# Optimization experiments

Hardware: AMD Instinct MI355X
Metric: run time of the kernel (lower is better)

The kernel has to match this reference:

```python
import jax, jax.numpy as jnp
import numpy as np

N_QUBITS = 4
DIM = 16  # 2**4 amplitudes
VOCAB = 40
SEQ = 1048576

# PennyLane default.qubit: wire 0 is the most-significant bit of the basis index.
_BITS = np.array([[(b >> (N_QUBITS - 1 - q)) & 1 for q in range(N_QUBITS)]
                  for b in range(DIM)], dtype=np.int32)          # [16, 4]
_POPCNT = _BITS.sum(axis=1)                                      # [16] int
_ZSIGN = (1 - 2 * _BITS).astype(np.float32)                      # [16, 4], +1 for |0>, -1 for |1>

def _cnot_perm(c, t):
    # basis permutation of CNOT(control=c, target=t); it is an involution
    idx = np.arange(DIM)
    ctrl = (idx >> (N_QUBITS - 1 - c)) & 1
    flipped = idx ^ (1 << (N_QUBITS - 1 - t))
    return np.where(ctrl == 1, flipped, idx)

_PERMS = [_cnot_perm(i, i + 1) for i in range(N_QUBITS - 1)]  # CNOT(0,1),(1,2),(2,3)


def setup_inputs() -> dict:
    key = jax.random.key(0)
    k1, k2, k3 = jax.random.split(key, 3)
    x = jax.random.uniform(k1, (1, SEQ), dtype=jnp.float32)
    q_weights = 0.01 * jax.random.normal(k2, (N_QUBITS,), dtype=jnp.float32)
    fc_weight = jax.random.normal(k3, (VOCAB, N_QUBITS), dtype=jnp.float32) / jnp.sqrt(4.0)
    fc_bias = jnp.zeros((VOCAB,), dtype=jnp.float32)
    return {"x": x, "q_weights": q_weights, "fc_weight": fc_weight, "fc_bias": fc_bias}


def reference(x, q_weights, fc_weight, fc_bias):
    theta = x[0]                      # [S] per-token angle, same on all 4 wires
    c = jnp.cos(theta * 0.5)
    s = jnp.sin(theta * 0.5)
    one = jnp.ones_like(c)
    # powers c^k, s^k for k=0..4 (avoids pow-grad issues at 0)
    cpow = jnp.stack([one, c, c * c, c * c * c, c * c * c * c], axis=-1)  # [S,5]
    spow = jnp.stack([one, s, s * s, s * s * s, s * s * s * s], axis=-1)  # [S,5]
    # product state of RY(theta)|0> on each wire: amp_b = c^(4-popcnt) * s^popcnt
    state = cpow[:, N_QUBITS - _POPCNT] * spow[:, _POPCNT]               # [S,16] real
    # apply the CNOT chain (basis permutations)
    for p in _PERMS:
        state = state[:, p]
    # RZ(w_q) on each wire contributes phase exp(-i*w_q*z_q/2)
    zs = jnp.asarray(_ZSIGN)                                              # [16,4]
    phase = jnp.exp(-0.5j * (zs @ q_weights.astype(jnp.float32)))         # [16] complex
    psi = state.astype(jnp.complex64) * phase                             # [S,16]
    probs = jnp.real(psi * jnp.conj(psi))                                 # [S,16]
    expvals = probs @ zs                                                  # [S,4] <Z_q>
    return expvals @ fc_weight.T + fc_bias                                # [S,VOCAB]
```

## Files before the change

kernel.cpp:

```cpp
#include <hip/hip_runtime.h>

#define THREADS 256

__global__ __launch_bounds__(THREADS) void sqm_kernel(
    const float* __restrict__ x,
    const float* __restrict__ fcw,
    const float* __restrict__ fcb,
    float* __restrict__ out,
    int n)
{
    const int Z[5][4] = {
        { 1, 1, 1, 1},
        { 2, 0,-2,-4},
        { 0,-2, 0, 6},
        {-2, 0, 2,-4},
        {-1, 1,-1, 1},
    };

    __shared__ __align__(16) float sA[5][40];
    __shared__ __align__(16) float sB[40];
    __shared__ float sU[THREADS * 5];

    const int t = threadIdx.x;

    if (t < 200) {
        const int k = t / 40, v = t % 40;
        float a = 0.f;
        #pragma unroll
        for (int q = 0; q < 4; ++q) a += (float)Z[k][q] * fcw[v * 4 + q];
        sA[k][v] = a;
    } else if (t < 240) {
        sB[t - 200] = fcb[t - 200];
    }

    const long long base = (long long)blockIdx.x * THREADS;
    const int i = (int)(base + t);
    const float theta = (i < n) ? x[i] : 0.f;
    const float C = 0.5f + 0.5f * __cosf(theta);
    const float S = 1.f - C;
    const float C2 = C * C, S2 = S * S, CS = C * S;
    sU[t * 5 + 0] = C2 * C2;
    sU[t * 5 + 1] = C2 * CS;
    sU[t * 5 + 2] = CS * CS;
    sU[t * 5 + 3] = CS * S2;
    sU[t * 5 + 4] = S2 * S2;
    __syncthreads();

    float4* __restrict__ out4 = reinterpret_cast<float4*>(out);
    const long long blockF4 = (long long)blockIdx.x * (THREADS * 10);
    const long long totalF4 = (long long)n * 10;
    #pragma unroll
    for (int kk = 0; kk < 10; ++kk) {
        const int j = t + kk * THREADS;
        const long long gj = blockF4 + j;
        if (gj < totalF4) {
            const int row = j / 10;
            const int c4  = (j - row * 10) * 4;
            const float u0 = sU[row * 5 + 0];
            const float u1 = sU[row * 5 + 1];
            const float u2 = sU[row * 5 + 2];
            const float u3 = sU[row * 5 + 3];
            const float u4 = sU[row * 5 + 4];
            const float4 a0 = *reinterpret_cast<const float4*>(&sA[0][c4]);
            const float4 a1 = *reinterpret_cast<const float4*>(&sA[1][c4]);
            const float4 a2 = *reinterpret_cast<const float4*>(&sA[2][c4]);
            const float4 a3 = *reinterpret_cast<const float4*>(&sA[3][c4]);
            const float4 a4 = *reinterpret_cast<const float4*>(&sA[4][c4]);
            const float4 b  = *reinterpret_cast<const float4*>(&sB[c4]);
            float4 r;
            r.x = b.x + u0*a0.x + u1*a1.x + u2*a2.x + u3*a3.x + u4*a4.x;
            r.y = b.y + u0*a0.y + u1*a1.y + u2*a2.y + u3*a3.y + u4*a4.y;
            r.z = b.z + u0*a0.z + u1*a1.z + u2*a2.z + u3*a3.z + u4*a4.z;
            r.w = b.w + u0*a0.w + u1*a1.w + u2*a2.w + u3*a3.w + u4*a4.w;
            out4[gj] = r;
        }
    }
}

extern "C" void kernel_launch(void* const* d_in, const int* in_sizes, int n_in,
                              void* d_out, int out_size, void* d_ws, size_t ws_size,
                              hipStream_t stream) {
    const float* x   = (const float*)d_in[0];
    const float* fcw = (const float*)d_in[2];
    const float* fcb = (const float*)d_in[3];
    float* out = (float*)d_out;
    const int n = in_sizes[0];
    const int grid = (n + THREADS - 1) / THREADS;
    hipLaunchKernelGGL(sqm_kernel, dim3(grid), dim3(THREADS), 0, stream,
                       x, fcw, fcb, out, n);
}
```

Baseline: 173.2 us.

## Vectorize per-row coefficient LDS layout, share sA loads across paired outputs, use nontemporal stores

Stores the five per-token coefficients as one 16-byte vector plus a separate scalar so each row needs two LDS reads instead of five. The output loop is restructured so each iteration handles two output float4s that share the same column (5*256 float4 apart is exactly 128 rows), letting the sA/sB loads be reused, and the per-element division is replaced by incremental row/column tracking. Output writes switch to nontemporal stores to avoid polluting cache for the large streaming output. This adds some index bookkeeping, and it depends on the pairing arithmetic staying correct.

```diff
diff --git a/kernel.cpp b/kernel.cpp
--- a/kernel.cpp
+++ b/kernel.cpp
@@ -1,6 +1,8 @@
 #include <hip/hip_runtime.h>
 
 #define THREADS 256
+
+typedef float f32x4 __attribute__((ext_vector_type(4)));
 
 __global__ __launch_bounds__(THREADS) void sqm_kernel(
     const float* __restrict__ x,
@@ -17,9 +19,10 @@
         {-1, 1,-1, 1},
     };
 
-    __shared__ __align__(16) float sA[5][40];
-    __shared__ __align__(16) float sB[40];
-    __shared__ float sU[THREADS * 5];
+    __shared__ __align__(16) float  sA[5][40];
+    __shared__ __align__(16) float  sB[40];
+    __shared__ __align__(16) f32x4  sU4[THREADS];
+    __shared__ float                sU5[THREADS];
 
     const int t = threadIdx.x;
 
@@ -39,41 +42,45 @@
     const float C = 0.5f + 0.5f * __cosf(theta);
     const float S = 1.f - C;
     const float C2 = C * C, S2 = S * S, CS = C * S;
-    sU[t * 5 + 0] = C2 * C2;
-    sU[t * 5 + 1] = C2 * CS;
-    sU[t * 5 + 2] = CS * CS;
-    sU[t * 5 + 3] = CS * S2;
-    sU[t * 5 + 4] = S2 * S2;
+    sU4[t] = (f32x4){C2 * C2, C2 * CS, CS * CS, CS * S2};
+    sU5[t] = S2 * S2;
     __syncthreads();
 
-    float4* __restrict__ out4 = reinterpret_cast<float4*>(out);
+    f32x4* __restrict__ out4 = reinterpret_cast<f32x4*>(out);
     const long long blockF4 = (long long)blockIdx.x * (THREADS * 10);
     const long long totalF4 = (long long)n * 10;
+
+    int row = t / 10;
+    int m   = t - row * 10;
     #pragma unroll
-    for (int kk = 0; kk < 10; ++kk) {
-        const int j = t + kk * THREADS;
-        const long long gj = blockF4 + j;
-        if (gj < totalF4) {
-            const int row = j / 10;
-            const int c4  = (j - row * 10) * 4;
-            const float u0 = sU[row * 5 + 0];
-            const float u1 = sU[row * 5 + 1];
-            const float u2 = sU[row * 5 + 2];
-            const float u3 = sU[row * 5 + 3];
-            const float u4 = sU[row * 5 + 4];
-            const float4 a0 = *reinterpret_cast<const float4*>(&sA[0][c4]);
-            const float4 a1 = *reinterpret_cast<const float4*>(&sA[1][c4]);
-            const float4 a2 = *reinterpret_cast<const float4*>(&sA[2][c4]);
-            const float4 a3 = *reinterpret_cast<const float4*>(&sA[3][c4]);
-            const float4 a4 = *reinterpret_cast<const float4*>(&sA[4][c4]);
-            const float4 b  = *reinterpret_cast<const float4*>(&sB[c4]);
-            float4 r;
-            r.x = b.x + u0*a0.x + u1*a1.x + u2*a2.x + u3*a3.x + u4*a4.x;
-            r.y = b.y + u0*a0.y + u1*a1.y + u2*a2.y + u3*a3.y + u4*a4.y;
-            r.z = b.z + u0*a0.z + u1*a1.z + u2*a2.z + u3*a3.z + u4*a4.z;
-            r.w = b.w + u0*a0.w + u1*a1.w + u2*a2.w + u3*a3.w + u4*a4.w;
-            out4[gj] = r;
+    for (int p = 0; p < 5; ++p) {
+        const int c4 = m * 4;
+        const long long gj0 = blockF4 + t + p * THREADS;
+        const long long gj1 = gj0 + 5 * THREADS;
+        const int rA = row, rB = row + 128;
+
+        const f32x4 a0 = *reinterpret_cast<const f32x4*>(&sA[0][c4]);
+        const f32x4 a1 = *reinterpret_cast<const f32x4*>(&sA[1][c4]);
+        const f32x4 a2 = *reinterpret_cast<const f32x4*>(&sA[2][c4]);
+        const f32x4 a3 = *reinterpret_cast<const f32x4*>(&sA[3][c4]);
+        const f32x4 a4 = *reinterpret_cast<const f32x4*>(&sA[4][c4]);
+        const f32x4 b  = *reinterpret_cast<const f32x4*>(&sB[c4]);
+
+        {
+            const f32x4 u = sU4[rA];
+            const float u4 = sU5[rA];
+            f32x4 r = b + u.x*a0 + u.y*a1 + u.z*a2 + u.w*a3 + u4*a4;
+            if (gj0 < totalF4) __builtin_nontemporal_store(r, out4 + gj0);
         }
+        {
+            const f32x4 u = sU4[rB];
+            const float u4 = sU5[rB];
+            f32x4 r = b + u.x*a0 + u.y*a1 + u.z*a2 + u.w*a3 + u4*a4;
+            if (gj1 < totalF4) __builtin_nontemporal_store(r, out4 + gj1);
+        }
+
+        row += 25; m += 6;
+        if (m >= 10) { m -= 10; row += 1; }
     }
 }
 
```

New measurement: 182.3 us. 5.3% more time.

## Rewrite output as Horner polynomial in S with 320-thread blocks

Applied to the files above, without the earlier changes.

Re-expresses the logits as a degree-4 polynomial in S = sin^2(theta/2), so each thread stores one scalar instead of five basis products and evaluates the result with Horner FMAs. The block size becomes 320, a multiple of 10 float4 chunks per row, so each thread keeps a fixed column group and loads its coefficients once, outside the loop. This removes the per-iteration divide/mod and the repeated LDS reads. The polynomial form can change rounding slightly, and 320 threads is five wave64s, which may affect occupancy.

```diff
diff --git a/kernel.cpp b/kernel.cpp
--- a/kernel.cpp
+++ b/kernel.cpp
@@ -1,6 +1,11 @@
 #include <hip/hip_runtime.h>
 
-#define THREADS 256
+#define THREADS 320
+#define ROWS_PER_BLOCK 320
+#define F4_PER_BLOCK 3200
+#define ITERS 10
+
+typedef float f32x4 __attribute__((ext_vector_type(4)));
 
 __global__ __launch_bounds__(THREADS) void sqm_kernel(
     const float* __restrict__ x,
@@ -9,71 +14,51 @@
     float* __restrict__ out,
     int n)
 {
-    const int Z[5][4] = {
-        { 1, 1, 1, 1},
-        { 2, 0,-2,-4},
-        { 0,-2, 0, 6},
-        {-2, 0, 2,-4},
-        {-1, 1,-1, 1},
-    };
-
-    __shared__ __align__(16) float sA[5][40];
-    __shared__ __align__(16) float sB[40];
-    __shared__ float sU[THREADS * 5];
+    __shared__ __align__(16) float sP[5][40];
+    __shared__ float sS[ROWS_PER_BLOCK];
 
     const int t = threadIdx.x;
 
-    if (t < 200) {
-        const int k = t / 40, v = t % 40;
-        float a = 0.f;
-        #pragma unroll
-        for (int q = 0; q < 4; ++q) a += (float)Z[k][q] * fcw[v * 4 + q];
-        sA[k][v] = a;
-    } else if (t < 240) {
-        sB[t - 200] = fcb[t - 200];
+    if (t < 40) {
+        const f32x4 w = *reinterpret_cast<const f32x4*>(&fcw[t * 4]);
+        const float b = fcb[t];
+        sP[0][t] = w.x + w.y + w.z + w.w + b;
+        sP[1][t] = -2.f*w.x - 4.f*w.y - 6.f*w.z - 8.f*w.w;
+        sP[2][t] =           4.f*w.y + 12.f*w.z + 24.f*w.w;
+        sP[3][t] =                     -8.f*w.z - 32.f*w.w;
+        sP[4][t] =                                16.f*w.w;
     }
 
-    const long long base = (long long)blockIdx.x * THREADS;
-    const int i = (int)(base + t);
+    const int i = blockIdx.x * ROWS_PER_BLOCK + t;
     const float theta = (i < n) ? x[i] : 0.f;
-    const float C = 0.5f + 0.5f * __cosf(theta);
-    const float S = 1.f - C;
-    const float C2 = C * C, S2 = S * S, CS = C * S;
-    sU[t * 5 + 0] = C2 * C2;
-    sU[t * 5 + 1] = C2 * CS;
-    sU[t * 5 + 2] = CS * CS;
-    sU[t * 5 + 3] = CS * S2;
-    sU[t * 5 + 4] = S2 * S2;
+    sS[t] = 0.5f - 0.5f * __cosf(theta);
     __syncthreads();
 
-    float4* __restrict__ out4 = reinterpret_cast<float4*>(out);
-    const long long blockF4 = (long long)blockIdx.x * (THREADS * 10);
+    const int m4 = (t % 10) * 4;
+    const f32x4 p0 = *reinterpret_cast<const f32x4*>(&sP[0][m4]);
+    const f32x4 p1 = *reinterpret_cast<const f32x4*>(&sP[1][m4]);
+    const f32x4 p2 = *reinterpret_cast<const f32x4*>(&sP[2][m4]);
+    const f32x4 p3 = *reinterpret_cast<const f32x4*>(&sP[3][m4]);
+    const f32x4 p4 = *reinterpret_cast<const f32x4*>(&sP[4][m4]);
+
+    f32x4* __restrict__ out4 = reinterpret_cast<f32x4*>(out);
+    const long long blockF4 = (long long)blockIdx.x * F4_PER_BLOCK;
     const long long totalF4 = (long long)n * 10;
+    int rloc = t / 10;
+
     #pragma unroll
-    for (int kk = 0; kk < 10; ++kk) {
-        const int j = t + kk * THREADS;
-        const long long gj = blockF4 + j;
+    for (int it = 0; it < ITERS; ++it) {
+        const long long gj = blockF4 + it * THREADS + t;
         if (gj < totalF4) {
-            const int row = j / 10;
-            const int c4  = (j - row * 10) * 4;
-            const float u0 = sU[row * 5 + 0];
-            const float u1 = sU[row * 5 + 1];
-            const float u2 = sU[row * 5 + 2];
-            const float u3 = sU[row * 5 + 3];
-            const float u4 = sU[row * 5 + 4];
-            const float4 a0 = *reinterpret_cast<const float4*>(&sA[0][c4]);
-            const float4 a1 = *reinterpret_cast<const float4*>(&sA[1][c4]);
-            const float4 a2 = *reinterpret_cast<const float4*>(&sA[2][c4]);
-            const float4 a3 = *reinterpret_cast<const float4*>(&sA[3][c4]);
-            const float4 a4 = *reinterpret_cast<const float4*>(&sA[4][c4]);
-            const float4 b  = *reinterpret_cast<const float4*>(&sB[c4]);
-            float4 r;
-            r.x = b.x + u0*a0.x + u1*a1.x + u2*a2.x + u3*a3.x + u4*a4.x;
-            r.y = b.y + u0*a0.y + u1*a1.y + u2*a2.y + u3*a3.y + u4*a4.y;
-            r.z = b.z + u0*a0.z + u1*a1.z + u2*a2.z + u3*a3.z + u4*a4.z;
-            r.w = b.w + u0*a0.w + u1*a1.w + u2*a2.w + u3*a3.w + u4*a4.w;
+            const float S = sS[rloc];
+            f32x4 r = p4;
+            r = r * S + p3;
+            r = r * S + p2;
+            r = r * S + p1;
+            r = r * S + p0;
             out4[gj] = r;
         }
+        rloc += 32;
     }
 }
 
@@ -85,7 +70,7 @@
     const float* fcb = (const float*)d_in[3];
     float* out = (float*)d_out;
     const int n = in_sizes[0];
-    const int grid = (n + THREADS - 1) / THREADS;
+    const int grid = (n + ROWS_PER_BLOCK - 1) / ROWS_PER_BLOCK;
     hipLaunchKernelGGL(sqm_kernel, dim3(grid), dim3(THREADS), 0, stream,
                        x, fcw, fcb, out, n);
 }
```

New measurement: 171.4 us. No clear change (-1.0%).
